# Kernel optimization log

Hardware: AMD Instinct MI355X
Metric: run time of the kernel (lower is better)

The kernel has to match this reference:

```python
import jax, jax.numpy as jnp
import numpy as np

N_NODES = 50000
N_EDGES = 600000
N_GRAPHS = 512
IN_C, HID_C, OUT_C = 128, 128, 64


def setup_inputs() -> dict:
    key = jax.random.key(0)
    ks = jax.random.split(key, 16)
    inp = {
        "x": jax.random.normal(ks[0], (N_NODES, IN_C), dtype=jnp.float32),
        "edge_index": jax.random.randint(ks[1], (2, N_EDGES), 0, N_NODES, dtype=jnp.int64),
        "batch": jnp.sort(jax.random.randint(ks[2], (N_NODES,), 0, N_GRAPHS, dtype=jnp.int64)),
    }
    # GINConv MLPs: Linear(din,dout) -> ReLU -> Linear(dout,dout)
    dims = [(IN_C, HID_C), (HID_C, HID_C), (HID_C, OUT_C)]
    ki = 3
    for l, (din, dout) in enumerate(dims):
        inp[f"w1_{l}"] = jax.random.normal(ks[ki], (din, dout), jnp.float32) / np.sqrt(din).astype(np.float32)
        inp[f"b1_{l}"] = jnp.zeros((dout,), jnp.float32)
        inp[f"w2_{l}"] = jax.random.normal(ks[ki + 1], (dout, dout), jnp.float32) / np.sqrt(dout).astype(np.float32)
        inp[f"b2_{l}"] = jnp.zeros((dout,), jnp.float32)
        ki += 2
    return inp


def _gin_conv(x, src, dst, w1, b1, w2, b2):
    # sum-aggregate neighbor features: agg[i] = sum_{(j->i) in E} x[j]
    agg = jax.ops.segment_sum(x[src], dst, num_segments=N_NODES)
    h = x + agg  # eps = 0 -> (1+eps)*x + agg
    h = jnp.maximum(h @ w1 + b1, 0.0)
    return h @ w2 + b2


def reference(x, edge_index, batch,
              w1_0, b1_0, w2_0, b2_0,
              w1_1, b1_1, w2_1, b2_1,
              w1_2, b1_2, w2_2, b2_2):
    src, dst = edge_index[0], edge_index[1]
    params = [(w1_0, b1_0, w2_0, b2_0),
              (w1_1, b1_1, w2_1, b2_1),
              (w1_2, b1_2, w2_2, b2_2)]
    # first num_layers-1 convs with outer ReLU
    for l in range(2):
        x = jnp.maximum(_gin_conv(x, src, dst, *params[l]), 0.0)
    x = _gin_conv(x, src, dst, *params[2])
    # global_add_pool over graph ids -> [G, out_channels]
    return jax.ops.segment_sum(x, batch, num_segments=N_GRAPHS)
```

## Files before the change

kernel.cpp:

```cpp
#include <hip/hip_runtime.h>

#define N_NODES 50000
#define N_EDGES 600000
#define N_GRAPHS 512
#define CAP 48

typedef unsigned int u32;
typedef unsigned short u16;
typedef __attribute__((ext_vector_type(8))) short bf16x8;
typedef __attribute__((ext_vector_type(4))) float f32x4;

__device__ __forceinline__ float bflo(u32 v) { return __uint_as_float(v << 16); }
__device__ __forceinline__ float bfhi(u32 v) { return __uint_as_float(v & 0xffff0000u); }
__device__ __forceinline__ u16 f2bf(float f) {
    u32 x = __float_as_uint(f);
    return (u16)((x + 0x7fffu + ((x >> 16) & 1u)) >> 16);
}
__device__ __forceinline__ void addrow(float* a, uint4 v) {
    a[0] += bflo(v.x); a[1] += bfhi(v.x);
    a[2] += bflo(v.y); a[3] += bfhi(v.y);
    a[4] += bflo(v.z); a[5] += bfhi(v.z);
    a[6] += bflo(v.w); a[7] += bfhi(v.w);
}
__device__ __forceinline__ void addrow2(float* a, uint2 v) {
    a[0] += bflo(v.x); a[1] += bfhi(v.x);
    a[2] += bflo(v.y); a[3] += bfhi(v.y);
}

__device__ __forceinline__ int idx_at(const int* __restrict__ a, int i, int wide) {
    return wide ? a[2 * i] : a[i];
}

__global__ void init_kernel(const int* __restrict__ ei, int* __restrict__ cnt,
                            int* __restrict__ flag, float* __restrict__ out,
                            int out_n) {
    int i = blockIdx.x * 256 + threadIdx.x;
    if (i < N_NODES) cnt[i] = 0;
    if (i < out_n) out[i] = 0.f;
    if (blockIdx.x == 0 && threadIdx.x < 64) {
        int v = ei[2 * threadIdx.x + 1];
        unsigned long long nz = __ballot(v != 0);
        if (threadIdx.x == 0) *flag = (nz == 0ull) ? 1 : 0;
    }
}

struct CvtDesc { const float* w; u16* wt; int K, N, bx, bstart; };
struct CvtAll { CvtDesc d[6]; };
struct PrepArgs {
    const int* ei; const int* flag;
    int* cnt; int* slots;
    const float* x; u16* xb;
    CvtAll ca;
};
#define SCAT_B 2344
#define CVTX_B 6250
#define PREP_B (SCAT_B + CVTX_B + 76)

__global__ void prep_kernel(PrepArgs p) {
    int b = blockIdx.x;
    if (b < SCAT_B) {
        int e = b * 256 + threadIdx.x;
        if (e >= N_EDGES) return;
        int w = *p.flag;
        const int* src = p.ei;
        const int* dst = p.ei + (w ? 2 * N_EDGES : N_EDGES);
        int d = idx_at(dst, e, w);
        int pos = atomicAdd(&p.cnt[d], 1);
        if (pos < CAP) p.slots[d * CAP + pos] = idx_at(src, e, w);
        return;
    }
    if (b < SCAT_B + CVTX_B) {
        size_t i = (size_t)(b - SCAT_B) * 256 + threadIdx.x;
        float4 v = *(const float4*)&p.x[i * 4];
        u32 o0 = (u32)f2bf(v.x) | ((u32)f2bf(v.y) << 16);
        u32 o1 = (u32)f2bf(v.z) | ((u32)f2bf(v.w) << 16);
        uint2 o; o.x = o0; o.y = o1;
        *(uint2*)&p.xb[i * 4] = o;
        return;
    }
    __shared__ float tile[32][33];
    int rel0 = b - (SCAT_B + CVTX_B);
    int di = 0;
#pragma unroll
    for (int i = 1; i < 6; ++i) if (rel0 >= p.ca.d[i].bstart) di = i;
    CvtDesc d = p.ca.d[di];
    int rel = rel0 - d.bstart;
    int bk = (rel % d.bx) * 32, bn = (rel / d.bx) * 32;
    int tx = threadIdx.x & 31, ty = threadIdx.x >> 5;
#pragma unroll
    for (int yy = 0; yy < 32; yy += 8)
        tile[ty + yy][tx] = d.w[(size_t)(bk + ty + yy) * d.N + bn + tx];
    __syncthreads();
#pragma unroll
    for (int yy = 0; yy < 32; yy += 8)
        d.wt[(size_t)(bn + ty + yy) * d.K + bk + tx] = f2bf(tile[tx][ty + yy]);
}

template <int RELU_OUT, int CHAIN>
__global__ __launch_bounds__(1024) void fused_layer(
    const u16* __restrict__ xb, const int* __restrict__ cnt,
    const int* __restrict__ slots,
    const u16* __restrict__ w1t, const float* __restrict__ b1,
    const u16* __restrict__ w2t, const float* __restrict__ b2,
    const u16* __restrict__ w3t, u16* __restrict__ zout,
    u16* __restrict__ yout)
{
    __shared__ __attribute__((aligned(16))) char smemA[64 * 128 * 2];
    __shared__ __attribute__((aligned(16))) u16 ts[64 * 128];
    u16* hs = (u16*)smemA;
    u16* ybt = (u16*)smemA;

    const int tid = threadIdx.x;
    const int wave = tid >> 6, lane = tid & 63;
    const int g = lane >> 4;
    const int l = lane & 15;
    const int base = blockIdx.x * 64;

    {
        int rr = wave * 4 + g;
        int node = base + rr;
        if (node < N_NODES) {
            uint4 sv = *(const uint4*)(xb + ((size_t)node << 7) + l * 8);
            float acc[8] = { bflo(sv.x), bfhi(sv.x), bflo(sv.y), bfhi(sv.y),
                             bflo(sv.z), bfhi(sv.z), bflo(sv.w), bfhi(sv.w) };
            int deg = cnt[node]; if (deg > CAP) deg = CAP;
            const int* sp = slots + node * CAP;
            int j = 0;
            for (; j + 4 <= deg; j += 4) {
                int s0 = sp[j], s1 = sp[j + 1], s2 = sp[j + 2], s3 = sp[j + 3];
                uint4 v0 = *(const uint4*)(xb + ((size_t)s0 << 7) + l * 8);
                uint4 v1 = *(const uint4*)(xb + ((size_t)s1 << 7) + l * 8);
                uint4 v2 = *(const uint4*)(xb + ((size_t)s2 << 7) + l * 8);
                uint4 v3 = *(const uint4*)(xb + ((size_t)s3 << 7) + l * 8);
                addrow(acc, v0); addrow(acc, v1);
                addrow(acc, v2); addrow(acc, v3);
            }
            for (; j < deg; ++j) {
                int s0 = sp[j];
                uint4 v0 = *(const uint4*)(xb + ((size_t)s0 << 7) + l * 8);
                addrow(acc, v0);
            }
            uint4 o;
            o.x = (u32)f2bf(acc[0]) | ((u32)f2bf(acc[1]) << 16);
            o.y = (u32)f2bf(acc[2]) | ((u32)f2bf(acc[3]) << 16);
            o.z = (u32)f2bf(acc[4]) | ((u32)f2bf(acc[5]) << 16);
            o.w = (u32)f2bf(acc[6]) | ((u32)f2bf(acc[7]) << 16);
            int c = (l * 8) ^ ((rr & 7) << 3);
            *(uint4*)&hs[rr * 128 + c] = o;
        }
    }
    __syncthreads();

    const int m = lane & 15;
    const int ko = (lane >> 4) * 8;
    const int rb = (wave & 3) * 16;
    const int cbase = (wave >> 2) * 32;

    {
        const int rr = rb + m;
        const int sw = (rr & 7) << 3;
        bf16x8 a1[4];
#pragma unroll
        for (int s = 0; s < 4; ++s)
            a1[s] = *(const bf16x8*)&hs[rr * 128 + ((s * 32 + ko) ^ sw)];
        f32x4 acc[2];
#pragma unroll
        for (int nt = 0; nt < 2; ++nt) acc[nt] = (f32x4){0.f, 0.f, 0.f, 0.f};
#pragma unroll
        for (int nt = 0; nt < 2; ++nt) {
            int n = cbase + nt * 16 + m;
#pragma unroll
            for (int s = 0; s < 4; ++s) {
                bf16x8 bf = *(const bf16x8*)&w1t[(size_t)n * 128 + s * 32 + ko];
                acc[nt] = __builtin_amdgcn_mfma_f32_16x16x32_bf16(a1[s], bf, acc[nt], 0, 0, 0);
            }
        }
#pragma unroll
        for (int nt = 0; nt < 2; ++nt) {
            int n = cbase + nt * 16 + m;
            float bias = b1[n];
#pragma unroll
            for (int j2 = 0; j2 < 4; ++j2) {
                int dr = rb + (lane >> 4) * 4 + j2;
                float v = fmaxf(acc[nt][j2] + bias, 0.f);
                ts[dr * 128 + (n ^ ((dr & 7) << 3))] = f2bf(v);
            }
        }
    }
    __syncthreads();

    {
        const int rr = rb + m;
        const int sw = (rr & 7) << 3;
        bf16x8 a2[4];
#pragma unroll
        for (int s = 0; s < 4; ++s)
            a2[s] = *(const bf16x8*)&ts[rr * 128 + ((s * 32 + ko) ^ sw)];
        f32x4 acc[2];
#pragma unroll
        for (int nt = 0; nt < 2; ++nt) acc[nt] = (f32x4){0.f, 0.f, 0.f, 0.f};
#pragma unroll
        for (int nt = 0; nt < 2; ++nt) {
            int n = cbase + nt * 16 + m;
#pragma unroll
            for (int s = 0; s < 4; ++s) {
                bf16x8 bf = *(const bf16x8*)&w2t[(size_t)n * 128 + s * 32 + ko];
                acc[nt] = __builtin_amdgcn_mfma_f32_16x16x32_bf16(a2[s], bf, acc[nt], 0, 0, 0);
            }
        }
        if (CHAIN) {
#pragma unroll
            for (int nt = 0; nt < 2; ++nt) {
                int n = cbase + nt * 16 + m;
                float bias = b2[n];
#pragma unroll
                for (int j2 = 0; j2 < 4; ++j2) {
                    int dr = rb + (lane >> 4) * 4 + j2;
                    float v = fmaxf(acc[nt][j2] + bias, 0.f);
                    ybt[dr * 128 + (n ^ ((dr & 7) << 3))] = f2bf(v);
                }
            }
        } else {
#pragma unroll
            for (int nt = 0; nt < 2; ++nt) {
                int n = cbase + nt * 16 + m;
                float bias = b2[n];
#pragma unroll
                for (int j2 = 0; j2 < 4; ++j2) {
                    int dr = rb + (lane >> 4) * 4 + j2;
                    int node = base + dr;
                    if (node < N_NODES) {
                        float v = acc[nt][j2] + bias;
                        if (RELU_OUT) v = fmaxf(v, 0.f);
                        yout[(size_t)node * 128 + n] = f2bf(v);
                    }
                }
            }
        }
    }
    if (CHAIN) {
        __syncthreads();
        const int rr = rb + m;
        const int sw = (rr & 7) << 3;
        const int cb3 = (wave >> 2) * 16;
        bf16x8 a3[4];
#pragma unroll
        for (int s = 0; s < 4; ++s)
            a3[s] = *(const bf16x8*)&ybt[rr * 128 + ((s * 32 + ko) ^ sw)];
        f32x4 acc3 = (f32x4){0.f, 0.f, 0.f, 0.f};
        int n3 = cb3 + m;
#pragma unroll
        for (int s = 0; s < 4; ++s) {
            bf16x8 bf = *(const bf16x8*)&w3t[(size_t)n3 * 128 + s * 32 + ko];
            acc3 = __builtin_amdgcn_mfma_f32_16x16x32_bf16(a3[s], bf, acc3, 0, 0, 0);
        }
#pragma unroll
        for (int j2 = 0; j2 < 4; ++j2) {
            int dr = rb + (lane >> 4) * 4 + j2;
            int node = base + dr;
            if (node < N_NODES)
                zout[(size_t)node * 64 + n3] = f2bf(acc3[j2]);
        }
    }
}

__global__ __launch_bounds__(1024) void fused_last(
    const u16* __restrict__ z, const int* __restrict__ cnt,
    const int* __restrict__ slots,
    const float* __restrict__ b1, const u16* __restrict__ w2t,
    const float* __restrict__ b2,
    const int* __restrict__ batch, const int* __restrict__ flagp,
    float* __restrict__ out)
{
    constexpr int YB_ST = 66;
    __shared__ __attribute__((aligned(16))) char smemA[64 * YB_ST * 4];
    __shared__ int gids[64];
    u16* hs = (u16*)smemA;
    float* yb = (float*)smemA;

    const int tid = threadIdx.x;
    const int wave = tid >> 6, lane = tid & 63;
    const int g = lane >> 4;
    const int l = lane & 15;
    const int base = blockIdx.x * 64;
    const int wflag = *flagp;

    if (tid < 64) {
        int node = base + tid;
        gids[tid] = (node < N_NODES) ? idx_at(batch, node, wflag) : -1;
    }

    {
        int rr = wave * 4 + g;
        int node = base + rr;
        if (node < N_NODES) {
            uint2 sv = *(const uint2*)(z + ((size_t)node << 6) + l * 4);
            float acc[4] = { bflo(sv.x), bfhi(sv.x), bflo(sv.y), bfhi(sv.y) };
            int deg = cnt[node]; if (deg > CAP) deg = CAP;
            const int* sp = slots + node * CAP;
            int j = 0;
            for (; j + 4 <= deg; j += 4) {
                int s0 = sp[j], s1 = sp[j + 1], s2 = sp[j + 2], s3 = sp[j + 3];
                uint2 v0 = *(const uint2*)(z + ((size_t)s0 << 6) + l * 4);
                uint2 v1 = *(const uint2*)(z + ((size_t)s1 << 6) + l * 4);
                uint2 v2 = *(const uint2*)(z + ((size_t)s2 << 6) + l * 4);
                uint2 v3 = *(const uint2*)(z + ((size_t)s3 << 6) + l * 4);
                addrow2(acc, v0); addrow2(acc, v1);
                addrow2(acc, v2); addrow2(acc, v3);
            }
            for (; j < deg; ++j) {
                int s0 = sp[j];
                uint2 v0 = *(const uint2*)(z + ((size_t)s0 << 6) + l * 4);
                addrow2(acc, v0);
            }
            float t0 = fmaxf(acc[0] + b1[l * 4 + 0], 0.f);
            float t1 = fmaxf(acc[1] + b1[l * 4 + 1], 0.f);
            float t2 = fmaxf(acc[2] + b1[l * 4 + 2], 0.f);
            float t3 = fmaxf(acc[3] + b1[l * 4 + 3], 0.f);
            uint2 o;
            o.x = (u32)f2bf(t0) | ((u32)f2bf(t1) << 16);
            o.y = (u32)f2bf(t2) | ((u32)f2bf(t3) << 16);
            int c = (l * 4) ^ ((rr & 7) << 3);
            *(uint2*)&hs[rr * 64 + c] = o;
        }
    }
    __syncthreads();

    const int m = lane & 15;
    const int ko = (lane >> 4) * 8;
    const int rb = (wave & 3) * 16;
    const int cb = (wave >> 2) * 16;

    {
        const int rr = rb + m;
        const int sw = (rr & 7) << 3;
        bf16x8 a2[2];
#pragma unroll
        for (int s = 0; s < 2; ++s)
            a2[s] = *(const bf16x8*)&hs[rr * 64 + ((s * 32 + ko) ^ sw)];
        f32x4 acc = (f32x4){0.f, 0.f, 0.f, 0.f};
        int n = cb + m;
#pragma unroll
        for (int s = 0; s < 2; ++s) {
            bf16x8 bf = *(const bf16x8*)&w2t[(size_t)n * 64 + s * 32 + ko];
            acc = __builtin_amdgcn_mfma_f32_16x16x32_bf16(a2[s], bf, acc, 0, 0, 0);
        }
        float bias = b2[n];
        __syncthreads();
#pragma unroll
        for (int j2 = 0; j2 < 4; ++j2) {
            int dr = rb + (lane >> 4) * 4 + j2;
            yb[dr * YB_ST + n] = acc[j2] + bias;
        }
    }
    __syncthreads();

    {
        int gl = gids[lane];
        int gp = (lane > 0) ? gids[lane - 1] : gl;
        unsigned long long mask = __ballot(lane > 0 && gl != gp) | 1ull;
        int nruns = (int)__popcll(mask);
        int c = tid >> 4, s = tid & 15;
        unsigned long long mm = mask;
        for (int r = 0; r < nruns; ++r) {
            int start = (int)__builtin_ctzll(mm);
            mm &= mm - 1;
            int end = mm ? (int)__builtin_ctzll(mm) : 64;
            int gid = gids[start];
            if (gid >= 0) {
                float sum = 0.f;
                for (int n2 = start + s; n2 < end; n2 += 16)
                    sum += yb[n2 * YB_ST + c];
                sum += __shfl_xor(sum, 1);
                sum += __shfl_xor(sum, 2);
                sum += __shfl_xor(sum, 4);
                sum += __shfl_xor(sum, 8);
                if (s == 0)
                    atomicAdd(&out[(size_t)gid * 64 + c], sum);
            }
        }
    }
}

extern "C" void kernel_launch(void* const* d_in, const int* in_sizes, int n_in,
                              void* d_out, int out_size, void* d_ws, size_t ws_size,
                              hipStream_t stream) {
    const float* x     = (const float*)d_in[0];
    const int*   ei    = (const int*)d_in[1];
    const int*   batch = (const int*)d_in[2];
    const float* w1[3] = {(const float*)d_in[3], (const float*)d_in[7],  (const float*)d_in[11]};
    const float* b1[3] = {(const float*)d_in[4], (const float*)d_in[8],  (const float*)d_in[12]};
    const float* w2[3] = {(const float*)d_in[5], (const float*)d_in[9],  (const float*)d_in[13]};
    const float* b2[3] = {(const float*)d_in[6], (const float*)d_in[10], (const float*)d_in[14]};
    float* out = (float*)d_out;

    char* ws = (char*)d_ws;
    int*   cnt     = (int*)(ws + 0);
    int*   flag    = (int*)(ws + 200704);
    int*   slots   = (int*)(ws + 201728);
    u16*   xb      = (u16*)(ws + 9801728);
    u16*   yA      = (u16*)(ws + 22601728);
    u16*   wts     = (u16*)(ws + 35401728);
    u16*   zbuf    = xb;
    u16* w1t0 = wts +      0;
    u16* w2t0 = wts +  16384;
    u16* w1t1 = wts +  32768;
    u16* w2t1 = wts +  49152;
    u16* w1t2 = wts +  65536;
    u16* w2t2 = wts +  73728;

    init_kernel<<<196, 256, 0, stream>>>(ei, cnt, flag, out, out_size);

    PrepArgs pa;
    pa.ei = ei; pa.flag = flag; pa.cnt = cnt; pa.slots = slots;
    pa.x = x; pa.xb = xb;
    pa.ca.d[0] = {w1[0], w1t0, 128, 128, 4,  0};
    pa.ca.d[1] = {w2[0], w2t0, 128, 128, 4, 16};
    pa.ca.d[2] = {w1[1], w1t1, 128, 128, 4, 32};
    pa.ca.d[3] = {w2[1], w2t1, 128, 128, 4, 48};
    pa.ca.d[4] = {w1[2], w1t2, 128,  64, 4, 64};
    pa.ca.d[5] = {w2[2], w2t2,  64,  64, 2, 72};
    prep_kernel<<<PREP_B, 256, 0, stream>>>(pa);

    const int NBK = (N_NODES + 63) / 64;
    fused_layer<1, 0><<<NBK, 1024, 0, stream>>>(xb, cnt, slots, w1t0, b1[0],
                                                w2t0, b2[0], (const u16*)0,
                                                (u16*)0, yA);
    fused_layer<1, 1><<<NBK, 1024, 0, stream>>>(yA, cnt, slots, w1t1, b1[1],
                                                w2t1, b2[1], w1t2, zbuf,
                                                (u16*)0);
    fused_last<<<NBK, 1024, 0, stream>>>(zbuf, cnt, slots, b1[2], w2t2, b2[2],
                                         batch, flag, out);
}
```

Before: 197.6 us.

## Split fused gather+MLP layers into separate small-block aggregation and MLP kernels

Each fused layer kernel (neighbor gather-sum followed by MFMA MLP in one 1024-thread block) is split into a 256-thread aggregation kernel that writes the aggregated bf16 rows to a global buffer, and a separate MLP/pool kernel that loads them into swizzled shared memory. The aim is better latency hiding and occupancy for the irregular gather, which previously ran inside large blocks held up by the MLP's shared-memory footprint. The cost is three extra kernel launches and an extra global write and read of the aggregated features per layer. The MLP tile load now reads rows past N_NODES without a bounds check, so it relies on workspace padding.

```diff
diff --git a/kernel.cpp b/kernel.cpp
--- a/kernel.cpp
+++ b/kernel.cpp
@@ -66,7 +66,7 @@
         const int* dst = p.ei + (w ? 2 * N_EDGES : N_EDGES);
         int d = idx_at(dst, e, w);
         int pos = atomicAdd(&p.cnt[d], 1);
-        if (pos < CAP) p.slots[d * CAP + pos] = idx_at(src, e, w);
+        if (pos < CAP) p.slots[(size_t)d * CAP + pos] = idx_at(src, e, w);
         return;
     }
     if (b < SCAT_B + CVTX_B) {
@@ -96,58 +96,94 @@
         d.wt[(size_t)(bn + ty + yy) * d.K + bk + tx] = f2bf(tile[tx][ty + yy]);
 }
 
-template <int RELU_OUT, int CHAIN>
-__global__ __launch_bounds__(1024) void fused_layer(
-    const u16* __restrict__ xb, const int* __restrict__ cnt,
-    const int* __restrict__ slots,
+__global__ void agg128_kernel(const u16* __restrict__ xb, const int* __restrict__ cnt,
+                              const int* __restrict__ slots, u16* __restrict__ h) {
+    int node = blockIdx.x * 16 + (threadIdx.x >> 4);
+    int l = threadIdx.x & 15;
+    if (node >= N_NODES) return;
+    uint4 sv = *(const uint4*)(xb + ((size_t)node << 7) + l * 8);
+    float acc[8] = { bflo(sv.x), bfhi(sv.x), bflo(sv.y), bfhi(sv.y),
+                     bflo(sv.z), bfhi(sv.z), bflo(sv.w), bfhi(sv.w) };
+    int deg = cnt[node]; if (deg > CAP) deg = CAP;
+    const int* sp = slots + (size_t)node * CAP;
+    int j = 0;
+    for (; j + 4 <= deg; j += 4) {
+        int s0 = sp[j], s1 = sp[j + 1], s2 = sp[j + 2], s3 = sp[j + 3];
+        uint4 v0 = *(const uint4*)(xb + ((size_t)s0 << 7) + l * 8);
+        uint4 v1 = *(const uint4*)(xb + ((size_t)s1 << 7) + l * 8);
+        uint4 v2 = *(const uint4*)(xb + ((size_t)s2 << 7) + l * 8);
+        uint4 v3 = *(const uint4*)(xb + ((size_t)s3 << 7) + l * 8);
+        addrow(acc, v0); addrow(acc, v1);
+        addrow(acc, v2); addrow(acc, v3);
+    }
+    for (; j < deg; ++j) {
+        int s0 = sp[j];
+        uint4 v0 = *(const uint4*)(xb + ((size_t)s0 << 7) + l * 8);
+        addrow(acc, v0);
+    }
+    uint4 o;
+    o.x = (u32)f2bf(acc[0]) | ((u32)f2bf(acc[1]) << 16);
+    o.y = (u32)f2bf(acc[2]) | ((u32)f2bf(acc[3]) << 16);
+    o.z = (u32)f2bf(acc[4]) | ((u32)f2bf(acc[5]) << 16);
+    o.w = (u32)f2bf(acc[6]) | ((u32)f2bf(acc[7]) << 16);
+    *(uint4*)(h + ((size_t)node << 7) + l * 8) = o;
+}
+
+__global__ void agg64_kernel(const u16* __restrict__ z, const int* __restrict__ cnt,
+                             const int* __restrict__ slots,
+                             const float* __restrict__ b1, u16* __restrict__ tout) {
+    int node = blockIdx.x * 16 + (threadIdx.x >> 4);
+    int l = threadIdx.x & 15;
+    if (node >= N_NODES) return;
+    uint2 sv = *(const uint2*)(z + ((size_t)node << 6) + l * 4);
+    float acc[4] = { bflo(sv.x), bfhi(sv.x), bflo(sv.y), bfhi(sv.y) };
+    int deg = cnt[node]; if (deg > CAP) deg = CAP;
+    const int* sp = slots + (size_t)node * CAP;
+    int j = 0;
+    for (; j + 4 <= deg; j += 4) {
+        int s0 = sp[j], s1 = sp[j + 1], s2 = sp[j + 2], s3 = sp[j + 3];
+        uint2 v0 = *(const uint2*)(z + ((size_t)s0 << 6) + l * 4);
+        uint2 v1 = *(const uint2*)(z + ((size_t)s1 << 6) + l * 4);
+        uint2 v2 = *(const uint2*)(z + ((size_t)s2 << 6) + l * 4);
+        uint2 v3 = *(const uint2*)(z + ((size_t)s3 << 6) + l * 4);
+        addrow2(acc, v0); addrow2(acc, v1);
+        addrow2(acc, v2); addrow2(acc, v3);
+    }
+    for (; j < deg; ++j) {
+        int s0 = sp[j];
+        uint2 v0 = *(const uint2*)(z + ((size_t)s0 << 6) + l * 4);
+        addrow2(acc, v0);
+    }
+    float t0 = fmaxf(acc[0] + b1[l * 4 + 0], 0.f);
+    float t1 = fmaxf(acc[1] + b1[l * 4 + 1], 0.f);
+    float t2 = fmaxf(acc[2] + b1[l * 4 + 2], 0.f);
+    float t3 = fmaxf(acc[3] + b1[l * 4 + 3], 0.f);
+    uint2 o;
+    o.x = (u32)f2bf(t0) | ((u32)f2bf(t1) << 16);
+    o.y = (u32)f2bf(t2) | ((u32)f2bf(t3) << 16);
+    *(uint2*)(tout + ((size_t)node << 6) + l * 4) = o;
+}
+
+template <int CHAIN>
+__global__ __launch_bounds__(1024) void mlp_kernel(
+    const u16* __restrict__ h,
     const u16* __restrict__ w1t, const float* __restrict__ b1,
     const u16* __restrict__ w2t, const float* __restrict__ b2,
     const u16* __restrict__ w3t, u16* __restrict__ zout,
     u16* __restrict__ yout)
 {
-    __shared__ __attribute__((aligned(16))) char smemA[64 * 128 * 2];
+    __shared__ __attribute__((aligned(16))) u16 hs[64 * 128];
     __shared__ __attribute__((aligned(16))) u16 ts[64 * 128];
-    u16* hs = (u16*)smemA;
-    u16* ybt = (u16*)smemA;
+    u16* ybt = hs;
 
     const int tid = threadIdx.x;
     const int wave = tid >> 6, lane = tid & 63;
-    const int g = lane >> 4;
-    const int l = lane & 15;
     const int base = blockIdx.x * 64;
 
     {
-        int rr = wave * 4 + g;
-        int node = base + rr;
-        if (node < N_NODES) {
-            uint4 sv = *(const uint4*)(xb + ((size_t)node << 7) + l * 8);
-            float acc[8] = { bflo(sv.x), bfhi(sv.x), bflo(sv.y), bfhi(sv.y),
-                             bflo(sv.z), bfhi(sv.z), bflo(sv.w), bfhi(sv.w) };
-            int deg = cnt[node]; if (deg > CAP) deg = CAP;
-            const int* sp = slots + node * CAP;
-            int j = 0;
-            for (; j + 4 <= deg; j += 4) {
-                int s0 = sp[j], s1 = sp[j + 1], s2 = sp[j + 2], s3 = sp[j + 3];
-                uint4 v0 = *(const uint4*)(xb + ((size_t)s0 << 7) + l * 8);
-                uint4 v1 = *(const uint4*)(xb + ((size_t)s1 << 7) + l * 8);
-                uint4 v2 = *(const uint4*)(xb + ((size_t)s2 << 7) + l * 8);
-                uint4 v3 = *(const uint4*)(xb + ((size_t)s3 << 7) + l * 8);
-                addrow(acc, v0); addrow(acc, v1);
-                addrow(acc, v2); addrow(acc, v3);
-            }
-            for (; j < deg; ++j) {
-                int s0 = sp[j];
-                uint4 v0 = *(const uint4*)(xb + ((size_t)s0 << 7) + l * 8);
-                addrow(acc, v0);
-            }
-            uint4 o;
-            o.x = (u32)f2bf(acc[0]) | ((u32)f2bf(acc[1]) << 16);
-            o.y = (u32)f2bf(acc[2]) | ((u32)f2bf(acc[3]) << 16);
-            o.z = (u32)f2bf(acc[4]) | ((u32)f2bf(acc[5]) << 16);
-            o.w = (u32)f2bf(acc[6]) | ((u32)f2bf(acc[7]) << 16);
-            int c = (l * 8) ^ ((rr & 7) << 3);
-            *(uint4*)&hs[rr * 128 + c] = o;
-        }
+        int row = tid >> 4, cg = (tid & 15) * 8;
+        uint4 v = *(const uint4*)&h[((size_t)(base + row)) * 128 + cg];
+        *(uint4*)&hs[row * 128 + (cg ^ ((row & 7) << 3))] = v;
     }
     __syncthreads();
 
@@ -230,8 +266,7 @@
                     int dr = rb + (lane >> 4) * 4 + j2;
                     int node = base + dr;
                     if (node < N_NODES) {
-                        float v = acc[nt][j2] + bias;
-                        if (RELU_OUT) v = fmaxf(v, 0.f);
+                        float v = fmaxf(acc[nt][j2] + bias, 0.f);
                         yout[(size_t)node * 128 + n] = f2bf(v);
                     }
                 }
@@ -264,10 +299,8 @@
     }
 }
 
-__global__ __launch_bounds__(1024) void fused_last(
-    const u16* __restrict__ z, const int* __restrict__ cnt,
-    const int* __restrict__ slots,
-    const float* __restrict__ b1, const u16* __restrict__ w2t,
+__global__ __launch_bounds__(1024) void pool_kernel(
+    const u16* __restrict__ t, const u16* __restrict__ w2t,
     const float* __restrict__ b2,
     const int* __restrict__ batch, const int* __restrict__ flagp,
     float* __restrict__ out)
@@ -280,8 +313,6 @@
 
     const int tid = threadIdx.x;
     const int wave = tid >> 6, lane = tid & 63;
-    const int g = lane >> 4;
-    const int l = lane & 15;
     const int base = blockIdx.x * 64;
     const int wflag = *flagp;
 
@@ -289,40 +320,10 @@
         int node = base + tid;
         gids[tid] = (node < N_NODES) ? idx_at(batch, node, wflag) : -1;
     }
-
-    {
-        int rr = wave * 4 + g;
-        int node = base + rr;
-        if (node < N_NODES) {
-            uint2 sv = *(const uint2*)(z + ((size_t)node << 6) + l * 4);
-            float acc[4] = { bflo(sv.x), bfhi(sv.x), bflo(sv.y), bfhi(sv.y) };
-            int deg = cnt[node]; if (deg > CAP) deg = CAP;
-            const int* sp = slots + node * CAP;
-            int j = 0;
-            for (; j + 4 <= deg; j += 4) {
-                int s0 = sp[j], s1 = sp[j + 1], s2 = sp[j + 2], s3 = sp[j + 3];
-                uint2 v0 = *(const uint2*)(z + ((size_t)s0 << 6) + l * 4);
-                uint2 v1 = *(const uint2*)(z + ((size_t)s1 << 6) + l * 4);
-                uint2 v2 = *(const uint2*)(z + ((size_t)s2 << 6) + l * 4);
-                uint2 v3 = *(const uint2*)(z + ((size_t)s3 << 6) + l * 4);
-                addrow2(acc, v0); addrow2(acc, v1);
-                addrow2(acc, v2); addrow2(acc, v3);
-            }
-            for (; j < deg; ++j) {
-                int s0 = sp[j];
-                uint2 v0 = *(const uint2*)(z + ((size_t)s0 << 6) + l * 4);
-                addrow2(acc, v0);
-            }
-            float t0 = fmaxf(acc[0] + b1[l * 4 + 0], 0.f);
-            float t1 = fmaxf(acc[1] + b1[l * 4 + 1], 0.f);
-            float t2 = fmaxf(acc[2] + b1[l * 4 + 2], 0.f);
-            float t3 = fmaxf(acc[3] + b1[l * 4 + 3], 0.f);
-            uint2 o;
-            o.x = (u32)f2bf(t0) | ((u32)f2bf(t1) << 16);
-            o.y = (u32)f2bf(t2) | ((u32)f2bf(t3) << 16);
-            int c = (l * 4) ^ ((rr & 7) << 3);
-            *(uint2*)&hs[rr * 64 + c] = o;
-        }
+    {
+        int row = tid >> 4, c0 = (tid & 15) * 4;
+        uint2 v = *(const uint2*)&t[((size_t)(base + row)) * 64 + c0];
+        *(uint2*)&hs[row * 64 + (c0 ^ ((row & 7) << 3))] = v;
     }
     __syncthreads();
 
@@ -399,9 +400,11 @@
     int*   flag    = (int*)(ws + 200704);
     int*   slots   = (int*)(ws + 201728);
     u16*   xb      = (u16*)(ws + 9801728);
-    u16*   yA      = (u16*)(ws + 22601728);
-    u16*   wts     = (u16*)(ws + 35401728);
+    u16*   hbuf    = (u16*)(ws + 22601728);
+    u16*   yA      = (u16*)(ws + 35401728);
+    u16*   wts     = (u16*)(ws + 48201728);
     u16*   zbuf    = xb;
+    u16*   tbuf    = hbuf;
     u16* w1t0 = wts +      0;
     u16* w2t0 = wts +  16384;
     u16* w1t1 = wts +  32768;
@@ -422,13 +425,15 @@
     pa.ca.d[5] = {w2[2], w2t2,  64,  64, 2, 72};
     prep_kernel<<<PREP_B, 256, 0, stream>>>(pa);
 
-    const int NBK = (N_NODES + 63) / 64;
-    fused_layer<1, 0><<<NBK, 1024, 0, stream>>>(xb, cnt, slots, w1t0, b1[0],
-                                                w2t0, b2[0], (const u16*)0,
-                                                (u16*)0, yA);
-    fused_layer<1, 1><<<NBK, 1024, 0, stream>>>(yA, cnt, slots, w1t1, b1[1],
-                                                w2t1, b2[1], w1t2, zbuf,
-                                                (u16*)0);
-    fused_last<<<NBK, 1024, 0, stream>>>(zbuf, cnt, slots, b1[2], w2t2, b2[2],
-                                         batch, flag, out);
-}
+    const int NAGG = (N_NODES + 15) / 16;
+    const int NTIL = (N_NODES + 63) / 64;
+
+    agg128_kernel<<<NAGG, 256, 0, stream>>>(xb, cnt, slots, hbuf);
+    mlp_kernel<0><<<NTIL, 1024, 0, stream>>>(hbuf, w1t0, b1[0], w2t0, b2[0],
+                                             (const u16*)0, (u16*)0, yA);
+    agg128_kernel<<<NAGG, 256, 0, stream>>>(yA, cnt, slots, hbuf);
+    mlp_kernel<1><<<NTIL, 1024, 0, stream>>>(hbuf, w1t1, b1[1], w2t1, b2[1],
+                                             w1t2, zbuf, (u16*)0);
+    agg64_kernel<<<NAGG, 256, 0, stream>>>(zbuf, cnt, slots, b1[2], tbuf);
+    pool_kernel<<<NTIL, 1024, 0, stream>>>(tbuf, w2t2, b2[2], batch, flag, out);
+}
```

New measurement: 198.7 us. About the same (+0.6%).
